# Kernel optimization log

Measured on AMD Instinct MI355X. Metric: run time of the kernel, lower is better.

Reference implementation:

```python
import jax, jax.numpy as jnp
import numpy as np

NL, D, H, DH, DFF, DIN, MAXLEN = 3, 128, 4, 32, 512, 64, 4096
B, L = 2, 2048


def setup_inputs() -> dict:
    key = jax.random.key(0)
    ks = jax.random.split(key, 10)
    def n(k, shape, s=0.02):
        return jax.random.normal(k, shape, jnp.float32) * s
    return dict(
        x=jax.random.normal(ks[0], (B, L, DIN), jnp.float32),
        embed_w=n(ks[1], (D, DIN)), embed_b=jnp.zeros((D,), jnp.float32),
        pos_emb=n(ks[2], (MAXLEN + 1, D)),
        cls=n(ks[3], (1, 1, D)),
        in_proj_w=n(ks[4], (NL, 3 * D, D)), in_proj_b=jnp.zeros((NL, 3 * D), jnp.float32),
        out_w=n(ks[5], (NL, D, D)), out_b=jnp.zeros((NL, D), jnp.float32),
        ln1_s=jnp.ones((NL, D), jnp.float32), ln1_b=jnp.zeros((NL, D), jnp.float32),
        ln2_s=jnp.ones((NL, D), jnp.float32), ln2_b=jnp.zeros((NL, D), jnp.float32),
        ff1_w=n(ks[6], (NL, DFF, D)), ff1_b=jnp.zeros((NL, DFF), jnp.float32),
        ff2_w=n(ks[7], (NL, D, DFF)), ff2_b=jnp.zeros((NL, D), jnp.float32),
        head_ln_s=jnp.ones((D,), jnp.float32), head_ln_b=jnp.zeros((D,), jnp.float32),
        head_w=n(ks[8], (1, D)), head_b=jnp.zeros((1,), jnp.float32),
    )


def _ln(x, s, b, eps=1e-5):
    m = x.mean(-1, keepdims=True)
    v = ((x - m) ** 2).mean(-1, keepdims=True)
    return (x - m) * jax.lax.rsqrt(v + eps) * s + b


def reference(x, embed_w, embed_b, pos_emb, cls, in_proj_w, in_proj_b, out_w, out_b,
              ln1_s, ln1_b, ln2_s, ln2_b, ff1_w, ff1_b, ff2_w, ff2_b,
              head_ln_s, head_ln_b, head_w, head_b):
    b, l, _ = x.shape
    # token embedding + positional embeddings at indices 1..L (0 reserved for CLS)
    h = x @ embed_w.T + embed_b + pos_emb[1:l + 1]            # [B,L,D]
    cls_tok = jnp.broadcast_to(cls + pos_emb[0], (b, 1, D))   # CLS gets pos_emb[0]
    h = jnp.concatenate([cls_tok, h], axis=1)                 # [B,S,D], S=L+1
    s = l + 1
    scale = 1.0 / np.sqrt(DH).astype(np.float32)
    for i in range(NL):  # norm_first encoder layers, eager MHA (dropout=0 / eval)
        hn = _ln(h, ln1_s[i], ln1_b[i])
        qkv = hn @ in_proj_w[i].T + in_proj_b[i]
        q, k, v = jnp.split(qkv, 3, axis=-1)
        q = q.reshape(b, s, H, DH)
        k = k.reshape(b, s, H, DH)
        v = v.reshape(b, s, H, DH)
        attn = jax.nn.softmax(jnp.einsum('bqhd,bkhd->bhqk', q, k) * scale, axis=-1)
        o = jnp.einsum('bhqk,bkhd->bqhd', attn, v).reshape(b, s, D)
        h = h + o @ out_w[i].T + out_b[i]
        hn = _ln(h, ln2_s[i], ln2_b[i])
        h = h + jax.nn.relu(hn @ ff1_w[i].T + ff1_b[i]) @ ff2_w[i].T + ff2_b[i]
    pooled = _ln(h[:, 0], head_ln_s, head_ln_b)               # CLS pooling
    return (pooled @ head_w.T + head_b)[:, 0]                 # [B]
```

## Files before the change

kernel.cpp:

```cpp
#include <hip/hip_runtime.h>

typedef unsigned short u16;
typedef float f32x4 __attribute__((ext_vector_type(4)));
typedef short short8 __attribute__((ext_vector_type(8)));

#define S_LEN 2049
#define SPAD  2112
#define MP    4224
#define MT    264
#define KSPLIT 8

__device__ __forceinline__ float b2f(u16 u){
  unsigned int i = ((unsigned int)u) << 16; float f; __builtin_memcpy(&f, &i, 4); return f;
}
__device__ __forceinline__ u16 f2b(float f){
  unsigned int i; __builtin_memcpy(&i, &f, 4);
  unsigned int r = i + 0x7FFFu + ((i >> 16) & 1u);
  return (u16)(r >> 16);
}
__device__ __forceinline__ u16 f2b_fast(float f){
  unsigned int i; __builtin_memcpy(&i, &f, 4);
  return (u16)((i + 0x8000u) >> 16);
}
#if __has_builtin(__builtin_amdgcn_exp2f)
#define EXP2F(x) __builtin_amdgcn_exp2f(x)
#else
#define EXP2F(x) exp2f(x)
#endif

enum {
  OFF_X = 0,            OFF_EW = 262144,  OFF_EB = 270336,  OFF_POS = 270464,
  OFF_CLS = 794880,     OFF_IPW = 795008, OFF_IPB = 942464, OFF_OW = 943616,
  OFF_OB = 992768,      OFF_L1S = 993152, OFF_L1B = 993536, OFF_L2S = 993920,
  OFF_L2B = 994304,     OFF_F1W = 994688, OFF_F1B = 1191296, OFF_F2W = 1192832,
  OFF_F2B = 1389440,    OFF_HLS = 1389824, OFF_HLB = 1389952, OFF_HW = 1390080,
  OFF_HB = 1390208,     OFF_END = 1390209, CANON_PAD = 1390216
};

struct CArgs { const void* s[21]; };

__global__ __launch_bounds__(256) void init_kernel(
    CArgs a, u16* __restrict__ dst, float* __restrict__ h)
{
  const int offs[22] = {OFF_X,OFF_EW,OFF_EB,OFF_POS,OFF_CLS,OFF_IPW,OFF_IPB,OFF_OW,OFF_OB,
    OFF_L1S,OFF_L1B,OFF_L2S,OFF_L2B,OFF_F1W,OFF_F1B,OFF_F2W,OFF_F2B,OFF_HLS,OFF_HLB,
    OFF_HW,OFF_HB,OFF_END};
  int tid = blockIdx.x * 256 + threadIdx.x;
  if (tid < 256){
    int d = tid & 127, b = tid >> 7;
    h[(size_t)b * SPAD * 128 + d] =
        ((const float*)a.s[4])[d] + ((const float*)a.s[3])[d];
  }
  if (tid < 2 * 63 * 128){
    int b = tid / 8064, r = (tid % 8064) / 128, d = tid & 127;
    h[((size_t)b * SPAD + S_LEN + r) * 128 + d] = 0.f;
  }
  if (tid >= OFF_END) return;
  int lo = 0, hi = 21;
  while (hi - lo > 1){ int mid = (lo + hi) >> 1; if (tid >= offs[mid]) lo = mid; else hi = mid; }
  dst[tid] = f2b(((const float*)a.s[lo])[tid - offs[lo]]);
}

__global__ __launch_bounds__(256) void embed_kernel(const u16* __restrict__ cw, float* __restrict__ h)
{
  int lane = threadIdx.x & 63;
  int wave = blockIdx.x * 4 + (threadIdx.x >> 6);
  int mt = wave >> 3, nt = wave & 7;
  int mi = lane & 15, quad = lane >> 4;
  const u16* Ap = cw + OFF_X + (size_t)(mt * 16 + mi) * 64 + quad * 8;
  const u16* Wp = cw + OFF_EW + (size_t)(nt * 16 + mi) * 64 + quad * 8;
  f32x4 acc = {0.f, 0.f, 0.f, 0.f};
#pragma unroll
  for (int kc = 0; kc < 2; kc++){
    short8 av = *(const short8*)(Ap + kc * 32);
    short8 wv = *(const short8*)(Wp + kc * 32);
    acc = __builtin_amdgcn_mfma_f32_16x16x32_bf16(av, wv, acc, 0, 0, 0);
  }
  int n = nt * 16 + mi;
  float ebv = b2f(cw[OFF_EB + n]);
#pragma unroll
  for (int r = 0; r < 4; r++){
    int m = mt * 16 + quad * 4 + r;
    int b = m >> 11, s = (m & 2047) + 1;
    h[((size_t)b * SPAD + s) * 128 + n] =
        acc[r] + ebv + b2f(cw[OFF_POS + (size_t)s * 128 + n]);
  }
}

template<int N, int MODE>
__global__ __launch_bounds__(256, 4) void lngemm_kernel(
    const float* __restrict__ h,
    const u16* __restrict__ g, const u16* __restrict__ be,
    const u16* __restrict__ W, const u16* __restrict__ bias, u16* __restrict__ out)
{
  constexpr int NT = N / 16;
  int lane = threadIdx.x & 63;
  int wave = blockIdx.x * 4 + (threadIdx.x >> 6);
  int mt = wave / NT, nt = wave - mt * NT;
  int mi = lane & 15, quad = lane >> 4;
  const float* hrow = h + (size_t)(mt * 16 + mi) * 128 + quad * 8;
  float v[32];
  float sm = 0.f;
#pragma unroll
  for (int kc = 0; kc < 4; kc++){
    f32x4 x0 = *(const f32x4*)(hrow + kc * 32);
    f32x4 x1 = *(const f32x4*)(hrow + kc * 32 + 4);
#pragma unroll
    for (int j = 0; j < 4; j++){ v[kc*8+j] = x0[j]; v[kc*8+4+j] = x1[j]; }
    sm += x0[0]+x0[1]+x0[2]+x0[3]+x1[0]+x1[1]+x1[2]+x1[3];
  }
  sm += __shfl_xor(sm, 16, 64); sm += __shfl_xor(sm, 32, 64);
  float mean = sm * (1.f/128.f);
  float vv = 0.f;
#pragma unroll
  for (int j = 0; j < 32; j++){ float d = v[j] - mean; vv += d * d; }
  vv += __shfl_xor(vv, 16, 64); vv += __shfl_xor(vv, 32, 64);
  float rstd = rsqrtf(vv * (1.f/128.f) + 1e-5f);
  short8 af[4];
#pragma unroll
  for (int kc = 0; kc < 4; kc++){
    short8 gs = *(const short8*)(g  + kc * 32 + quad * 8);
    short8 bs = *(const short8*)(be + kc * 32 + quad * 8);
#pragma unroll
    for (int j = 0; j < 8; j++)
      af[kc][j] = (short)f2b((v[kc*8+j] - mean) * rstd * b2f((u16)gs[j]) + b2f((u16)bs[j]));
  }
  const u16* Wp = W + (size_t)(nt * 16 + mi) * 128 + quad * 8;
  f32x4 acc = {0.f, 0.f, 0.f, 0.f};
#pragma unroll
  for (int kc = 0; kc < 4; kc++){
    short8 wv = *(const short8*)(Wp + kc * 32);
    acc = __builtin_amdgcn_mfma_f32_16x16x32_bf16(af[kc], wv, acc, 0, 0, 0);
  }
  int n = nt * 16 + mi;
  float bv = b2f(bias[n]);
#pragma unroll
  for (int r = 0; r < 4; r++){
    int m = mt * 16 + quad * 4 + r;
    float val = acc[r] + bv;
    if (MODE == 0){
      int which = n >> 7, d = n & 127, hd = d >> 5, dh = d & 31;
      int b_ = (m >= SPAD) ? 1 : 0;
      int s  = m - b_ * SPAD;
      out[(size_t)(((which * 2 + b_) * 4 + hd) * SPAD + s) * 32 + dh] = f2b(val);
    } else {
      out[(size_t)m * N + n] = f2b(val > 0.f ? val : 0.f);
    }
  }
}

template<int K>
__global__ __launch_bounds__(256) void gemm_res_kernel(
    const u16* __restrict__ A, const u16* __restrict__ W, const u16* __restrict__ bias,
    float* __restrict__ hres)
{
  int lane = threadIdx.x & 63;
  int wave = blockIdx.x * 4 + (threadIdx.x >> 6);
  int mt = wave >> 3, nt = wave & 7;
  int mi = lane & 15, quad = lane >> 4;
  const u16* Ap = A + (size_t)(mt * 16 + mi) * K + quad * 8;
  const u16* Wp = W + (size_t)(nt * 16 + mi) * K + quad * 8;
  f32x4 acc = {0.f, 0.f, 0.f, 0.f};
#pragma unroll
  for (int kc = 0; kc < K / 32; kc++){
    short8 a = *(const short8*)(Ap + kc * 32);
    short8 b = *(const short8*)(Wp + kc * 32);
    acc = __builtin_amdgcn_mfma_f32_16x16x32_bf16(a, b, acc, 0, 0, 0);
  }
  int n = nt * 16 + mi;
  float bv = b2f(bias[n]);
#pragma unroll
  for (int r = 0; r < 4; r++){
    int m = mt * 16 + quad * 4 + r;
    hres[(size_t)m * 128 + n] += acc[r] + bv;
  }
}

__global__ __launch_bounds__(256, 4) void attn_kernel(
    const u16* __restrict__ qkv, float* __restrict__ Opart, float* __restrict__ Lpart)
{
  __shared__ u16 Kl[64 * 40];
  __shared__ u16 Vt[32 * 72];
  __shared__ u16 Pl[4][16 * 72];
  int tid = threadIdx.x;
  int lane = tid & 63, w = tid >> 6;
  int qt = blockIdx.x, bh = blockIdx.y, split = blockIdx.z;
  const u16* Qb = qkv + (size_t)bh * SPAD * 32;
  const u16* Kb = qkv + (size_t)(8 + bh) * SPAD * 32;
  const u16* Vb = qkv + (size_t)(16 + bh) * SPAD * 32;
  int mi = lane & 15, quad = lane >> 4;
  int q0 = qt * 64 + w * 16;
  short8 qf = *(const short8*)(Qb + (size_t)(q0 + mi) * 32 + quad * 8);
  f32x4 o0 = {0,0,0,0}, o1 = {0,0,0,0};
  float lp[4] = {0.f, 0.f, 0.f, 0.f};
  int c0 = (split * 33) >> 3, c1 = ((split + 1) * 33) >> 3;
  int kkey = tid >> 2, kdh = (tid & 3) * 8;
  int vdh = tid & 31, vgrp = tid >> 5;
  u16* Pw = Pl[w];
  short8 kreg = *(const short8*)(Kb + (size_t)(c0 * 64 + kkey) * 32 + kdh);
  ushort4 va, vb;
  {
    const u16* vp = Vb + (size_t)(c0 * 64 + vgrp * 4) * 32 + vdh;
    va.x = vp[0];    va.y = vp[32];   va.z = vp[64];   va.w = vp[96];
    vb.x = vp[1024]; vb.y = vp[1056]; vb.z = vp[1088]; vb.w = vp[1120];
  }
  for (int c = c0; c < c1; c++){
    __syncthreads();
    *(short8*)&Kl[kkey * 40 + kdh] = kreg;
    *(ushort4*)&Vt[vdh * 72 + vgrp * 4] = va;
    *(ushort4*)&Vt[vdh * 72 + (vgrp + 8) * 4] = vb;
    {
      int cn = (c + 1 < c1) ? c + 1 : c;
      kreg = *(const short8*)(Kb + (size_t)(cn * 64 + kkey) * 32 + kdh);
      const u16* vp = Vb + (size_t)(cn * 64 + vgrp * 4) * 32 + vdh;
      va.x = vp[0];    va.y = vp[32];   va.z = vp[64];   va.w = vp[96];
      vb.x = vp[1024]; vb.y = vp[1056]; vb.z = vp[1088]; vb.w = vp[1120];
    }
    __syncthreads();
    int kb = c * 64;
#pragma unroll
    for (int kt = 0; kt < 4; kt++){
      short8 kf = *(const short8*)&Kl[(kt * 16 + mi) * 40 + quad * 8];
      f32x4 z = {0,0,0,0};
      f32x4 s = __builtin_amdgcn_mfma_f32_16x16x32_bf16(qf, kf, z, 0, 0, 0);
      bool val = (kb + kt * 16 + mi) < S_LEN;
#pragma unroll
      for (int r = 0; r < 4; r++){
        float p = val ? EXP2F(s[r] * 0.25503486f) : 0.f;
        lp[r] += p;
        Pw[(quad * 4 + r) * 72 + kt * 16 + mi] = f2b_fast(p);
      }
    }
    short8 pf0 = *(const short8*)&Pw[mi * 72 + quad * 8];
    short8 pf1 = *(const short8*)&Pw[mi * 72 + 32 + quad * 8];
    short8 wa0 = *(const short8*)&Vt[mi * 72 + quad * 8];
    short8 wa1 = *(const short8*)&Vt[mi * 72 + 32 + quad * 8];
    short8 wb0 = *(const short8*)&Vt[(16 + mi) * 72 + quad * 8];
    short8 wb1 = *(const short8*)&Vt[(16 + mi) * 72 + 32 + quad * 8];
    o0 = __builtin_amdgcn_mfma_f32_16x16x32_bf16(pf0, wa0, o0, 0, 0, 0);
    o0 = __builtin_amdgcn_mfma_f32_16x16x32_bf16(pf1, wa1, o0, 0, 0, 0);
    o1 = __builtin_amdgcn_mfma_f32_16x16x32_bf16(pf0, wb0, o1, 0, 0, 0);
    o1 = __builtin_amdgcn_mfma_f32_16x16x32_bf16(pf1, wb1, o1, 0, 0, 0);
  }
#pragma unroll
  for (int r = 0; r < 4; r++){
    lp[r] += __shfl_xor(lp[r], 1, 64); lp[r] += __shfl_xor(lp[r], 2, 64);
    lp[r] += __shfl_xor(lp[r], 4, 64); lp[r] += __shfl_xor(lp[r], 8, 64);
  }
  size_t pb = ((size_t)qt * 8 + bh) * KSPLIT + split;
  float* Ob = Opart + pb * 2048 + (size_t)w * 16 * 32;
#pragma unroll
  for (int r = 0; r < 4; r++){
    Ob[(quad * 4 + r) * 32 + mi]      = o0[r];
    Ob[(quad * 4 + r) * 32 + 16 + mi] = o1[r];
  }
  if (mi == 0){
#pragma unroll
    for (int r = 0; r < 4; r++)
      Lpart[pb * 64 + w * 16 + quad * 4 + r] = lp[r];
  }
}

__global__ __launch_bounds__(512, 2) void redout_kernel(
    const float* __restrict__ Opart, const float* __restrict__ Lpart,
    const u16* __restrict__ W, const u16* __restrict__ bias, float* __restrict__ hres)
{
  __shared__ u16 Al[16 * 136];
  int tid = threadIdx.x;
  int mt = blockIdx.x;
  int b = mt / 132, tle = mt % 132;
  int qt = tle >> 2, w = tle & 3;
  {
    int hd = tid >> 7;
    int e  = (tid * 4) & 511;
    int r  = e >> 5, dh0 = e & 31;
    size_t base = (((size_t)qt * 8 + (b * 4 + hd)) * KSPLIT) * 2048 + w * 512 + r * 32 + dh0;
    f32x4 acc = {0,0,0,0};
    float ls = 0.f;
#pragma unroll
    for (int sp = 0; sp < KSPLIT; sp++){
      acc += *(const f32x4*)(Opart + base + (size_t)sp * 2048);
      ls  += Lpart[(((size_t)qt * 8 + (b * 4 + hd)) * KSPLIT + sp) * 64 + w * 16 + r];
    }
    float inv = 1.f / fmaxf(ls, 1e-30f);
    ushort4 pk;
    pk.x = f2b(acc[0] * inv); pk.y = f2b(acc[1] * inv);
    pk.z = f2b(acc[2] * inv); pk.w = f2b(acc[3] * inv);
    *(ushort4*)&Al[r * 136 + hd * 32 + dh0] = pk;
  }
  __syncthreads();
  int lane = tid & 63, nt = tid >> 6;
  int mi = lane & 15, quad = lane >> 4;
  const u16* Wp = W + (size_t)(nt * 16 + mi) * 128 + quad * 8;
  f32x4 acc = {0.f, 0.f, 0.f, 0.f};
#pragma unroll
  for (int kc = 0; kc < 4; kc++){
    short8 af = *(const short8*)&Al[mi * 136 + kc * 32 + quad * 8];
    short8 wv = *(const short8*)(Wp + kc * 32);
    acc = __builtin_amdgcn_mfma_f32_16x16x32_bf16(af, wv, acc, 0, 0, 0);
  }
  int n = nt * 16 + mi;
  float bv = b2f(bias[n]);
#pragma unroll
  for (int r = 0; r < 4; r++){
    int m = mt * 16 + quad * 4 + r;
    hres[(size_t)m * 128 + n] += acc[r] + bv;
  }
}

__global__ __launch_bounds__(128) void head_kernel(
    const float* __restrict__ h, const u16* __restrict__ cw, float* __restrict__ out)
{
  __shared__ float red[128];
  int tid = threadIdx.x;
  for (int b = 0; b < 2; b++){
    float e = h[(size_t)b * SPAD * 128 + tid];
    red[tid] = e; __syncthreads();
    for (int st = 64; st > 0; st >>= 1){ if (tid < st) red[tid] += red[tid + st]; __syncthreads(); }
    float mean = red[0] * (1.f/128.f); __syncthreads();
    float d = e - mean; red[tid] = d * d; __syncthreads();
    for (int st = 64; st > 0; st >>= 1){ if (tid < st) red[tid] += red[tid + st]; __syncthreads(); }
    float rstd = rsqrtf(red[0] * (1.f/128.f) + 1e-5f); __syncthreads();
    float val = d * rstd * b2f(cw[OFF_HLS + tid]) + b2f(cw[OFF_HLB + tid]);
    red[tid] = val * b2f(cw[OFF_HW + tid]); __syncthreads();
    for (int st = 64; st > 0; st >>= 1){ if (tid < st) red[tid] += red[tid + st]; __syncthreads(); }
    if (tid == 0) out[b] = red[0] + b2f(cw[OFF_HB]);
    __syncthreads();
  }
}

extern "C" void kernel_launch(void* const* d_in, const int* in_sizes, int n_in,
                              void* d_out, int out_size, void* d_ws, size_t ws_size,
                              hipStream_t stream)
{
  char* ws = (char*)d_ws;
  u16* cw     = (u16*)ws;    ws += (size_t)CANON_PAD * 2;
  float* h    = (float*)ws;  ws += (size_t)MP * 128 * 4;
  u16* qkv    = (u16*)ws;    ws += (size_t)24 * SPAD * 32 * 2;
  u16* f1     = (u16*)ws;    ws += (size_t)MP * 512 * 2;
  float* Opart= (float*)ws;  ws += (size_t)33 * 8 * KSPLIT * 2048 * 4;
  float* Lpart= (float*)ws;  ws += (size_t)33 * 8 * KSPLIT * 64 * 4;

  CArgs ca;
  for (int i = 0; i < 21; i++) ca.s[i] = d_in[i];

  init_kernel<<<dim3((OFF_END + 255) / 256), dim3(256), 0, stream>>>(ca, cw, h);
  embed_kernel<<<dim3(512), dim3(256), 0, stream>>>(cw, h);
  for (int l = 0; l < 3; l++){
    lngemm_kernel<384, 0><<<dim3(MT * 24 / 4), dim3(256), 0, stream>>>(
        h, cw + OFF_L1S + l * 128, cw + OFF_L1B + l * 128,
        cw + OFF_IPW + (size_t)l * 384 * 128, cw + OFF_IPB + l * 384, qkv);
    attn_kernel<<<dim3(33, 8, KSPLIT), dim3(256), 0, stream>>>(qkv, Opart, Lpart);
    redout_kernel<<<dim3(MT), dim3(512), 0, stream>>>(
        Opart, Lpart, cw + OFF_OW + (size_t)l * 128 * 128, cw + OFF_OB + l * 128, h);
    lngemm_kernel<512, 2><<<dim3(MT * 32 / 4), dim3(256), 0, stream>>>(
        h, cw + OFF_L2S + l * 128, cw + OFF_L2B + l * 128,
        cw + OFF_F1W + (size_t)l * 512 * 128, cw + OFF_F1B + l * 512, f1);
    gemm_res_kernel<512><<<dim3(MT * 8 / 4), dim3(256), 0, stream>>>(
        f1, cw + OFF_F2W + (size_t)l * 128 * 512, cw + OFF_F2B + l * 128, h);
  }
  head_kernel<<<dim3(1), dim3(128), 0, stream>>>(h, cw, (float*)d_out);
}
```

Before: 319.2 us.

## Use 32x32 per-wave MFMA tiles in GEMMs and rebalance attention key splits

The LayerNorm-fused GEMMs and the FF2 residual GEMM now compute a 32x32 output tile per wave with four MFMA accumulators. This halves redundant LayerNorm recomputation and reuses A and W fragments across tiles. Attention key splitting rises from 8 to 11 so each split handles exactly 3 chunks, which adds more partial results for the reduction. The head kernel uses wave shuffles instead of shared-memory tree reductions. The larger tiles raise register pressure, and launch_bounds occupancy hints are dropped.

```diff
diff --git a/kernel.cpp b/kernel.cpp
--- a/kernel.cpp
+++ b/kernel.cpp
@@ -8,7 +8,8 @@
 #define SPAD  2112
 #define MP    4224
 #define MT    264
-#define KSPLIT 8
+#define MT32  132
+#define KSPLIT 11
 
 __device__ __forceinline__ float b2f(u16 u){
   unsigned int i = ((unsigned int)u) << 16; float f; __builtin_memcpy(&f, &i, 4); return f;
@@ -88,91 +89,119 @@
 }
 
 template<int N, int MODE>
-__global__ __launch_bounds__(256, 4) void lngemm_kernel(
+__global__ __launch_bounds__(256) void lngemm_kernel(
     const float* __restrict__ h,
     const u16* __restrict__ g, const u16* __restrict__ be,
     const u16* __restrict__ W, const u16* __restrict__ bias, u16* __restrict__ out)
 {
-  constexpr int NT = N / 16;
+  constexpr int NT = N / 32;
   int lane = threadIdx.x & 63;
   int wave = blockIdx.x * 4 + (threadIdx.x >> 6);
   int mt = wave / NT, nt = wave - mt * NT;
   int mi = lane & 15, quad = lane >> 4;
-  const float* hrow = h + (size_t)(mt * 16 + mi) * 128 + quad * 8;
-  float v[32];
-  float sm = 0.f;
+  short8 af[2][4];
+#pragma unroll
+  for (int gi = 0; gi < 2; gi++){
+    const float* hrow = h + (size_t)(mt * 32 + gi * 16 + mi) * 128 + quad * 8;
+    float v[32];
+    float sm = 0.f;
+#pragma unroll
+    for (int kc = 0; kc < 4; kc++){
+      f32x4 x0 = *(const f32x4*)(hrow + kc * 32);
+      f32x4 x1 = *(const f32x4*)(hrow + kc * 32 + 4);
+#pragma unroll
+      for (int j = 0; j < 4; j++){ v[kc*8+j] = x0[j]; v[kc*8+4+j] = x1[j]; }
+      sm += x0[0]+x0[1]+x0[2]+x0[3]+x1[0]+x1[1]+x1[2]+x1[3];
+    }
+    sm += __shfl_xor(sm, 16, 64); sm += __shfl_xor(sm, 32, 64);
+    float mean = sm * (1.f/128.f);
+    float vv = 0.f;
+#pragma unroll
+    for (int j = 0; j < 32; j++){ float d = v[j] - mean; vv += d * d; }
+    vv += __shfl_xor(vv, 16, 64); vv += __shfl_xor(vv, 32, 64);
+    float rstd = rsqrtf(vv * (1.f/128.f) + 1e-5f);
+#pragma unroll
+    for (int kc = 0; kc < 4; kc++){
+      short8 gs = *(const short8*)(g  + kc * 32 + quad * 8);
+      short8 bs = *(const short8*)(be + kc * 32 + quad * 8);
+#pragma unroll
+      for (int j = 0; j < 8; j++)
+        af[gi][kc][j] = (short)f2b((v[kc*8+j] - mean) * rstd * b2f((u16)gs[j]) + b2f((u16)bs[j]));
+    }
+  }
+  const u16* W0 = W + (size_t)(nt * 32 + mi) * 128 + quad * 8;
+  const u16* W1 = W0 + 16 * 128;
+  f32x4 a00 = {0,0,0,0}, a01 = {0,0,0,0}, a10 = {0,0,0,0}, a11 = {0,0,0,0};
 #pragma unroll
   for (int kc = 0; kc < 4; kc++){
-    f32x4 x0 = *(const f32x4*)(hrow + kc * 32);
-    f32x4 x1 = *(const f32x4*)(hrow + kc * 32 + 4);
-#pragma unroll
-    for (int j = 0; j < 4; j++){ v[kc*8+j] = x0[j]; v[kc*8+4+j] = x1[j]; }
-    sm += x0[0]+x0[1]+x0[2]+x0[3]+x1[0]+x1[1]+x1[2]+x1[3];
-  }
-  sm += __shfl_xor(sm, 16, 64); sm += __shfl_xor(sm, 32, 64);
-  float mean = sm * (1.f/128.f);
-  float vv = 0.f;
-#pragma unroll
-  for (int j = 0; j < 32; j++){ float d = v[j] - mean; vv += d * d; }
-  vv += __shfl_xor(vv, 16, 64); vv += __shfl_xor(vv, 32, 64);
-  float rstd = rsqrtf(vv * (1.f/128.f) + 1e-5f);
-  short8 af[4];
-#pragma unroll
-  for (int kc = 0; kc < 4; kc++){
-    short8 gs = *(const short8*)(g  + kc * 32 + quad * 8);
-    short8 bs = *(const short8*)(be + kc * 32 + quad * 8);
-#pragma unroll
-    for (int j = 0; j < 8; j++)
-      af[kc][j] = (short)f2b((v[kc*8+j] - mean) * rstd * b2f((u16)gs[j]) + b2f((u16)bs[j]));
-  }
-  const u16* Wp = W + (size_t)(nt * 16 + mi) * 128 + quad * 8;
-  f32x4 acc = {0.f, 0.f, 0.f, 0.f};
-#pragma unroll
-  for (int kc = 0; kc < 4; kc++){
-    short8 wv = *(const short8*)(Wp + kc * 32);
-    acc = __builtin_amdgcn_mfma_f32_16x16x32_bf16(af[kc], wv, acc, 0, 0, 0);
-  }
-  int n = nt * 16 + mi;
-  float bv = b2f(bias[n]);
-#pragma unroll
-  for (int r = 0; r < 4; r++){
-    int m = mt * 16 + quad * 4 + r;
-    float val = acc[r] + bv;
-    if (MODE == 0){
-      int which = n >> 7, d = n & 127, hd = d >> 5, dh = d & 31;
-      int b_ = (m >= SPAD) ? 1 : 0;
-      int s  = m - b_ * SPAD;
-      out[(size_t)(((which * 2 + b_) * 4 + hd) * SPAD + s) * 32 + dh] = f2b(val);
-    } else {
-      out[(size_t)m * N + n] = f2b(val > 0.f ? val : 0.f);
-    }
-  }
-}
-
-template<int K>
+    short8 w0 = *(const short8*)(W0 + kc * 32);
+    short8 w1 = *(const short8*)(W1 + kc * 32);
+    a00 = __builtin_amdgcn_mfma_f32_16x16x32_bf16(af[0][kc], w0, a00, 0, 0, 0);
+    a01 = __builtin_amdgcn_mfma_f32_16x16x32_bf16(af[0][kc], w1, a01, 0, 0, 0);
+    a10 = __builtin_amdgcn_mfma_f32_16x16x32_bf16(af[1][kc], w0, a10, 0, 0, 0);
+    a11 = __builtin_amdgcn_mfma_f32_16x16x32_bf16(af[1][kc], w1, a11, 0, 0, 0);
+  }
+#pragma unroll
+  for (int gi = 0; gi < 2; gi++){
+#pragma unroll
+    for (int wsel = 0; wsel < 2; wsel++){
+      f32x4 acc = gi ? (wsel ? a11 : a10) : (wsel ? a01 : a00);
+      int n = nt * 32 + wsel * 16 + mi;
+      float bv = b2f(bias[n]);
+#pragma unroll
+      for (int r = 0; r < 4; r++){
+        int m = mt * 32 + gi * 16 + quad * 4 + r;
+        float val = acc[r] + bv;
+        if (MODE == 0){
+          int which = n >> 7, d = n & 127, hd = d >> 5, dh = d & 31;
+          int b_ = (m >= SPAD) ? 1 : 0;
+          int s  = m - b_ * SPAD;
+          out[(size_t)(((which * 2 + b_) * 4 + hd) * SPAD + s) * 32 + dh] = f2b(val);
+        } else {
+          out[(size_t)m * N + n] = f2b(val > 0.f ? val : 0.f);
+        }
+      }
+    }
+  }
+}
+
 __global__ __launch_bounds__(256) void gemm_res_kernel(
     const u16* __restrict__ A, const u16* __restrict__ W, const u16* __restrict__ bias,
     float* __restrict__ hres)
 {
   int lane = threadIdx.x & 63;
   int wave = blockIdx.x * 4 + (threadIdx.x >> 6);
-  int mt = wave >> 3, nt = wave & 7;
-  int mi = lane & 15, quad = lane >> 4;
-  const u16* Ap = A + (size_t)(mt * 16 + mi) * K + quad * 8;
-  const u16* Wp = W + (size_t)(nt * 16 + mi) * K + quad * 8;
-  f32x4 acc = {0.f, 0.f, 0.f, 0.f};
-#pragma unroll
-  for (int kc = 0; kc < K / 32; kc++){
-    short8 a = *(const short8*)(Ap + kc * 32);
-    short8 b = *(const short8*)(Wp + kc * 32);
-    acc = __builtin_amdgcn_mfma_f32_16x16x32_bf16(a, b, acc, 0, 0, 0);
-  }
-  int n = nt * 16 + mi;
-  float bv = b2f(bias[n]);
-#pragma unroll
-  for (int r = 0; r < 4; r++){
-    int m = mt * 16 + quad * 4 + r;
-    hres[(size_t)m * 128 + n] += acc[r] + bv;
+  int mt = wave >> 2, nt = wave & 3;
+  int mi = lane & 15, quad = lane >> 4;
+  const u16* A0 = A + (size_t)(mt * 32 + mi) * 512 + quad * 8;
+  const u16* A1 = A0 + 16 * 512;
+  const u16* W0 = W + (size_t)(nt * 32 + mi) * 512 + quad * 8;
+  const u16* W1 = W0 + 16 * 512;
+  f32x4 a00 = {0,0,0,0}, a01 = {0,0,0,0}, a10 = {0,0,0,0}, a11 = {0,0,0,0};
+#pragma unroll
+  for (int kc = 0; kc < 16; kc++){
+    short8 x0 = *(const short8*)(A0 + kc * 32);
+    short8 x1 = *(const short8*)(A1 + kc * 32);
+    short8 w0 = *(const short8*)(W0 + kc * 32);
+    short8 w1 = *(const short8*)(W1 + kc * 32);
+    a00 = __builtin_amdgcn_mfma_f32_16x16x32_bf16(x0, w0, a00, 0, 0, 0);
+    a01 = __builtin_amdgcn_mfma_f32_16x16x32_bf16(x0, w1, a01, 0, 0, 0);
+    a10 = __builtin_amdgcn_mfma_f32_16x16x32_bf16(x1, w0, a10, 0, 0, 0);
+    a11 = __builtin_amdgcn_mfma_f32_16x16x32_bf16(x1, w1, a11, 0, 0, 0);
+  }
+#pragma unroll
+  for (int gi = 0; gi < 2; gi++){
+#pragma unroll
+    for (int wsel = 0; wsel < 2; wsel++){
+      f32x4 acc = gi ? (wsel ? a11 : a10) : (wsel ? a01 : a00);
+      int n = nt * 32 + wsel * 16 + mi;
+      float bv = b2f(bias[n]);
+#pragma unroll
+      for (int r = 0; r < 4; r++){
+        int m = mt * 32 + gi * 16 + quad * 4 + r;
+        hres[(size_t)m * 128 + n] += acc[r] + bv;
+      }
+    }
   }
 }
 
@@ -193,7 +222,7 @@
   short8 qf = *(const short8*)(Qb + (size_t)(q0 + mi) * 32 + quad * 8);
   f32x4 o0 = {0,0,0,0}, o1 = {0,0,0,0};
   float lp[4] = {0.f, 0.f, 0.f, 0.f};
-  int c0 = (split * 33) >> 3, c1 = ((split + 1) * 33) >> 3;
+  int c0 = split * 3, c1 = c0 + 3;
   int kkey = tid >> 2, kdh = (tid & 3) * 8;
   int vdh = tid & 31, vgrp = tid >> 5;
   u16* Pw = Pl[w];
@@ -274,13 +303,14 @@
     int hd = tid >> 7;
     int e  = (tid * 4) & 511;
     int r  = e >> 5, dh0 = e & 31;
-    size_t base = (((size_t)qt * 8 + (b * 4 + hd)) * KSPLIT) * 2048 + w * 512 + r * 32 + dh0;
+    size_t hb = ((size_t)qt * 8 + (b * 4 + hd)) * KSPLIT;
+    size_t base = hb * 2048 + w * 512 + r * 32 + dh0;
     f32x4 acc = {0,0,0,0};
     float ls = 0.f;
 #pragma unroll
     for (int sp = 0; sp < KSPLIT; sp++){
       acc += *(const f32x4*)(Opart + base + (size_t)sp * 2048);
-      ls  += Lpart[(((size_t)qt * 8 + (b * 4 + hd)) * KSPLIT + sp) * 64 + w * 16 + r];
+      ls  += Lpart[(hb + sp) * 64 + w * 16 + r];
     }
     float inv = 1.f / fmaxf(ls, 1e-30f);
     ushort4 pk;
@@ -308,24 +338,28 @@
   }
 }
 
-__global__ __launch_bounds__(128) void head_kernel(
+__global__ __launch_bounds__(64) void head_kernel(
     const float* __restrict__ h, const u16* __restrict__ cw, float* __restrict__ out)
 {
-  __shared__ float red[128];
-  int tid = threadIdx.x;
+  int lane = threadIdx.x;
   for (int b = 0; b < 2; b++){
-    float e = h[(size_t)b * SPAD * 128 + tid];
-    red[tid] = e; __syncthreads();
-    for (int st = 64; st > 0; st >>= 1){ if (tid < st) red[tid] += red[tid + st]; __syncthreads(); }
-    float mean = red[0] * (1.f/128.f); __syncthreads();
-    float d = e - mean; red[tid] = d * d; __syncthreads();
-    for (int st = 64; st > 0; st >>= 1){ if (tid < st) red[tid] += red[tid + st]; __syncthreads(); }
-    float rstd = rsqrtf(red[0] * (1.f/128.f) + 1e-5f); __syncthreads();
-    float val = d * rstd * b2f(cw[OFF_HLS + tid]) + b2f(cw[OFF_HLB + tid]);
-    red[tid] = val * b2f(cw[OFF_HW + tid]); __syncthreads();
-    for (int st = 64; st > 0; st >>= 1){ if (tid < st) red[tid] += red[tid + st]; __syncthreads(); }
-    if (tid == 0) out[b] = red[0] + b2f(cw[OFF_HB]);
-    __syncthreads();
+    float e0 = h[(size_t)b * SPAD * 128 + lane];
+    float e1 = h[(size_t)b * SPAD * 128 + 64 + lane];
+    float sm = e0 + e1;
+    sm += __shfl_xor(sm,1,64); sm += __shfl_xor(sm,2,64); sm += __shfl_xor(sm,4,64);
+    sm += __shfl_xor(sm,8,64); sm += __shfl_xor(sm,16,64); sm += __shfl_xor(sm,32,64);
+    float mean = sm * (1.f/128.f);
+    float d0 = e0 - mean, d1 = e1 - mean;
+    float vv = d0*d0 + d1*d1;
+    vv += __shfl_xor(vv,1,64); vv += __shfl_xor(vv,2,64); vv += __shfl_xor(vv,4,64);
+    vv += __shfl_xor(vv,8,64); vv += __shfl_xor(vv,16,64); vv += __shfl_xor(vv,32,64);
+    float rstd = rsqrtf(vv * (1.f/128.f) + 1e-5f);
+    float v0 = d0 * rstd * b2f(cw[OFF_HLS + lane])      + b2f(cw[OFF_HLB + lane]);
+    float v1 = d1 * rstd * b2f(cw[OFF_HLS + 64 + lane]) + b2f(cw[OFF_HLB + 64 + lane]);
+    float dot = v0 * b2f(cw[OFF_HW + lane]) + v1 * b2f(cw[OFF_HW + 64 + lane]);
+    dot += __shfl_xor(dot,1,64); dot += __shfl_xor(dot,2,64); dot += __shfl_xor(dot,4,64);
+    dot += __shfl_xor(dot,8,64); dot += __shfl_xor(dot,16,64); dot += __shfl_xor(dot,32,64);
+    if (lane == 0) out[b] = dot + b2f(cw[OFF_HB]);
   }
 }
 
@@ -347,17 +381,17 @@
   init_kernel<<<dim3((OFF_END + 255) / 256), dim3(256), 0, stream>>>(ca, cw, h);
   embed_kernel<<<dim3(512), dim3(256), 0, stream>>>(cw, h);
   for (int l = 0; l < 3; l++){
-    lngemm_kernel<384, 0><<<dim3(MT * 24 / 4), dim3(256), 0, stream>>>(
+    lngemm_kernel<384, 0><<<dim3(MT32 * 12 / 4), dim3(256), 0, stream>>>(
         h, cw + OFF_L1S + l * 128, cw + OFF_L1B + l * 128,
         cw + OFF_IPW + (size_t)l * 384 * 128, cw + OFF_IPB + l * 384, qkv);
     attn_kernel<<<dim3(33, 8, KSPLIT), dim3(256), 0, stream>>>(qkv, Opart, Lpart);
     redout_kernel<<<dim3(MT), dim3(512), 0, stream>>>(
         Opart, Lpart, cw + OFF_OW + (size_t)l * 128 * 128, cw + OFF_OB + l * 128, h);
-    lngemm_kernel<512, 2><<<dim3(MT * 32 / 4), dim3(256), 0, stream>>>(
+    lngemm_kernel<512, 2><<<dim3(MT32 * 16 / 4), dim3(256), 0, stream>>>(
         h, cw + OFF_L2S + l * 128, cw + OFF_L2B + l * 128,
         cw + OFF_F1W + (size_t)l * 512 * 128, cw + OFF_F1B + l * 512, f1);
-    gemm_res_kernel<512><<<dim3(MT * 8 / 4), dim3(256), 0, stream>>>(
+    gemm_res_kernel<<<dim3(MT32), dim3(256), 0, stream>>>(
         f1, cw + OFF_F2W + (size_t)l * 128 * 512, cw + OFF_F2B + l * 128, h);
   }
-  head_kernel<<<dim3(1), dim3(128), 0, stream>>>(h, cw, (float*)d_out);
-}
+  head_kernel<<<dim3(1), dim3(64), 0, stream>>>(h, cw, (float*)d_out);
+}
```

Measured after the change: 279.4 us. 1.14x faster.
